# Kernel optimization log

Hardware: AMD Instinct MI355X
Metric: run time of the kernel (lower is better)

## Reference

```python
import jax, jax.numpy as jnp
import numpy as np

B, T, F, G, H, N, C = 32, 64, 32, 32, 256, 20000, 32
EPS = 1e-5


def setup_inputs() -> dict:
    key = jax.random.key(0)
    ks = jax.random.split(key, 24)
    s = 0.05
    d = {}
    d["data_feats"] = jax.random.normal(ks[0], (B, T, F), jnp.float32)
    d["gat_output"] = jax.random.normal(ks[1], (B, N, G), jnp.float32)
    d["row_ids"] = jax.random.randint(ks[2], (B, T), 0, 2 * N, jnp.int32)
    d["node_ids"] = jax.random.randint(ks[3], (N,), 0, 2 * N, jnp.int32)
    # shared LSTM (2 layers): layer0 input F+G, layer1 input H; b = b_ih + b_hh fused
    d["shared_Wih0"] = jax.random.normal(ks[4], (4 * H, F + G)) * s
    d["shared_Whh0"] = jax.random.normal(ks[5], (4 * H, H)) * s
    d["shared_b0"] = jax.random.normal(ks[6], (4 * H,)) * s
    d["shared_Wih1"] = jax.random.normal(ks[7], (4 * H, H)) * s
    d["shared_Whh1"] = jax.random.normal(ks[8], (4 * H, H)) * s
    d["shared_b1"] = jax.random.normal(ks[9], (4 * H,)) * s
    # act/time/timeR LSTMs stacked on leading axis 3, each 2 layers of [4H,H]
    d["heads_Wih"] = jax.random.normal(ks[10], (3, 2, 4 * H, H)) * s
    d["heads_Whh"] = jax.random.normal(ks[11], (3, 2, 4 * H, H)) * s
    d["heads_b"] = jax.random.normal(ks[12], (3, 2, 4 * H)) * s
    d["bn_gnn_g"] = jnp.ones((G,), jnp.float32)
    d["bn_gnn_b"] = jnp.zeros((G,), jnp.float32)
    d["bn_shared_g"] = jnp.ones((H,), jnp.float32)
    d["bn_shared_b"] = jnp.zeros((H,), jnp.float32)
    d["heads_bn_g"] = jnp.ones((3, H), jnp.float32)
    d["heads_bn_b"] = jnp.zeros((3, H), jnp.float32)
    d["fc_act_W"] = jax.random.normal(ks[13], (C, H)) * s
    d["fc_act_b"] = jnp.zeros((C,), jnp.float32)
    d["fc_time_W"] = jax.random.normal(ks[14], (1, H)) * s
    d["fc_time_b"] = jnp.zeros((1,), jnp.float32)
    d["fc_timeR_W"] = jax.random.normal(ks[15], (1, H)) * s
    d["fc_timeR_b"] = jnp.zeros((1,), jnp.float32)
    return d


def batchnorm(x, gamma, beta):
    # BatchNorm1d training-mode: stats over (batch, length) per channel; x: [B, L, C]
    mean = jnp.mean(x, axis=(0, 1))
    var = jnp.var(x, axis=(0, 1))
    return (x - mean) * (gamma / jnp.sqrt(var + EPS)) + beta


def lstm_layer(x, Wih, Whh, b):
    # x: [B, T, Din]; PyTorch gate order i, f, g, o
    xp = jnp.einsum("btf,gf->btg", x, Wih) + b  # [B, T, 4H]
    h = Whh.shape[1]
    init = (jnp.zeros((x.shape[0], h), x.dtype), jnp.zeros((x.shape[0], h), x.dtype))

    def step(carry, xt):
        hprev, cprev = carry
        gates = xt + hprev @ Whh.T
        i, f, g, o = jnp.split(gates, 4, axis=-1)
        c = jax.nn.sigmoid(f) * cprev + jax.nn.sigmoid(i) * jnp.tanh(g)
        hnew = jax.nn.sigmoid(o) * jnp.tanh(c)
        return (hnew, c), hnew

    _, hs = jax.lax.scan(step, init, jnp.swapaxes(xp, 0, 1))
    return jnp.swapaxes(hs, 0, 1)  # [B, T, H]


def reference(data_feats, gat_output, row_ids, node_ids,
              shared_Wih0, shared_Whh0, shared_b0,
              shared_Wih1, shared_Whh1, shared_b1,
              heads_Wih, heads_Whh, heads_b,
              bn_gnn_g, bn_gnn_b, bn_shared_g, bn_shared_b,
              heads_bn_g, heads_bn_b,
              fc_act_W, fc_act_b, fc_time_W, fc_time_b, fc_timeR_W, fc_timeR_b):
    # --- graph branch: BN over GAT output, value-match lookup + gather ---
    gat_norm = batchnorm(gat_output, bn_gnn_g, bn_gnn_b)  # [B, N, G]
    eq = row_ids[:, :, None] == node_ids[None, None, :]   # [B, T, N]
    idx = jnp.argmax(eq, axis=-1)                          # first matching index
    found = jnp.any(eq, axis=-1)
    gathered = jnp.take_along_axis(gat_norm, idx[:, :, None], axis=1)  # [B, T, G]
    matched = jnp.where(found[:, :, None], gathered, 0.0)
    lstm_in = jnp.concatenate([data_feats, matched], axis=-1)  # [B, T, F+G]

    # --- shared 2-layer LSTM + BN (dropout off / eval) ---
    shared = lstm_layer(lstm_in, shared_Wih0, shared_Whh0, shared_b0)
    shared = lstm_layer(shared, shared_Wih1, shared_Whh1, shared_b1)
    shared = batchnorm(shared, bn_shared_g, bn_shared_b)

    # --- act / time / timeR head LSTMs (vmapped over the 3 heads) + BN ---
    def head(Wih, Whh, b, g, bb):
        hh = lstm_layer(shared, Wih[0], Whh[0], b[0])
        hh = lstm_layer(hh, Wih[1], Whh[1], b[1])
        return batchnorm(hh, g, bb)

    heads = jax.vmap(head)(heads_Wih, heads_Whh, heads_b, heads_bn_g, heads_bn_b)
    last = heads[:, :, -1, :]  # [3, B, H]

    act = jax.nn.softmax(last[0] @ fc_act_W.T + fc_act_b, axis=1)
    time = last[1] @ fc_time_W.T + fc_time_b
    timeR = last[2] @ fc_timeR_W.T + fc_timeR_b
    return act, time, timeR
```

## Files before the change

kernel.cpp:

```cpp
#include <hip/hip_runtime.h>
#include <hip/hip_fp16.h>
#include <math.h>

#define Bn 32
#define Tn 64
#define Fdim 32
#define Gdim 32
#define Hdim 256
#define Ndim 20000
#define Cdim 32
#define G4 1024
#define BT 2048
#define EPSc 1e-5f

__device__ __forceinline__ float sigmoidf_(float x){ return 1.0f/(1.0f + __expf(-x)); }
__device__ __forceinline__ float tanhf_(float x){ return 2.0f/(1.0f+__expf(-2.0f*x)) - 1.0f; }

typedef _Float16 h2t __attribute__((ext_vector_type(2)));

__device__ __forceinline__ float fdot2_(unsigned w, unsigned h, float acc){
#if defined(__has_builtin) && __has_builtin(__builtin_amdgcn_fdot2)
  return __builtin_amdgcn_fdot2(__builtin_bit_cast(h2t, w), __builtin_bit_cast(h2t, h), acc, false);
#else
  h2t a = __builtin_bit_cast(h2t, w), b = __builtin_bit_cast(h2t, h);
  acc = fmaf((float)a.x, (float)b.x, acc);
  return fmaf((float)a.y, (float)b.y, acc);
#endif
}

__device__ __forceinline__ unsigned packh_(float lo, float hi){
  unsigned ulo = (unsigned)__half_as_ushort(__float2half(lo));
  unsigned uhi = (unsigned)__half_as_ushort(__float2half(hi));
  return ulo | (uhi << 16);
}

__global__ void init_kernel(float* ws){
  int i = blockIdx.x*256 + threadIdx.x;
  if (i < 2112) ws[i] = 0.0f;
  int* table = (int*)(ws + 2112);
  if (i < 40000) table[i] = 0x7fffffff;
}

__global__ void bn_stats_kernel(const float* __restrict__ gat, float* __restrict__ sums){
  __shared__ float ss[256], sq[256];
  int tid = threadIdx.x;
  int idx = blockIdx.x*256 + tid;
  int stride = gridDim.x*256;
  const int total = Bn*Ndim*Gdim;
  float s=0.f,q=0.f;
  for (int i=idx; i<total; i+=stride){ float v = gat[i]; s+=v; q+=v*v; }
  ss[tid]=s; sq[tid]=q; __syncthreads();
  for (int off=128; off>=32; off>>=1){
    if(tid<off){ ss[tid]+=ss[tid+off]; sq[tid]+=sq[tid+off]; }
    __syncthreads();
  }
  if (tid<32){ atomicAdd(&sums[tid], ss[tid]); atomicAdd(&sums[32+tid], sq[tid]); }
}

__global__ void table_kernel(const int* __restrict__ node_ids, int* __restrict__ table){
  int i = blockIdx.x*256 + threadIdx.x;
  if (i < Ndim) atomicMin(&table[node_ids[i]], i);
}

__global__ void build_input_kernel(const float* __restrict__ feats, const float* __restrict__ gat,
    const int* __restrict__ row_ids, const int* __restrict__ table, const float* __restrict__ sums,
    const float* __restrict__ bng, const float* __restrict__ bnb, unsigned* __restrict__ out){
  int gt = blockIdx.x*256 + threadIdx.x;
  int pos = gt >> 5; int k2 = gt & 31;
  float lo, hi;
  if (k2 < 16){
    float2 v = *(const float2*)(feats + pos*Fdim + 2*k2);
    lo = v.x; hi = v.y;
  } else {
    int g0 = 2*(k2-16);
    int r = row_ids[pos];
    int idx = table[r];
    if (idx < Ndim){
      int b = pos / Tn;
      float2 x = *(const float2*)(gat + (size_t)(b*Ndim + idx)*Gdim + g0);
      const float cnt = (float)(Bn*Ndim);
      float m0 = sums[g0]/cnt,   v0 = sums[32+g0]/cnt - m0*m0;
      float m1 = sums[g0+1]/cnt, v1 = sums[32+g0+1]/cnt - m1*m1;
      lo = (x.x-m0)*bng[g0]*rsqrtf(v0+EPSc) + bnb[g0];
      hi = (x.y-m1)*bng[g0+1]*rsqrtf(v1+EPSc) + bnb[g0+1];
    } else { lo = 0.0f; hi = 0.0f; }
  }
  out[gt] = packh_(lo, hi);
}

struct TArgs { const float* src[8]; unsigned* dst[8]; int K[8]; };
__global__ void packwih_kernel(TArgs a){
  __shared__ unsigned tile[32][33];
  int mat = blockIdx.y;
  int K = a.K[mat];
  int K2 = K >> 1;
  int ktiles = K2 >> 5;
  int tk = blockIdx.x & 3;
  int tn = blockIdx.x >> 2;
  if (tk >= ktiles) return;
  const float* src = a.src[mat];
  unsigned* dst = a.dst[mat];
  int tx = threadIdx.x, ty = threadIdx.y;
  int n0 = tn*32, k2_0 = tk*32;
  #pragma unroll
  for (int i=0;i<4;i++){
    int nn = ty + 8*i;
    const float* p = src + (size_t)(n0+nn)*K + 2*(k2_0 + tx);
    tile[nn][tx] = packh_(p[0], p[1]);
  }
  __syncthreads();
  #pragma unroll
  for (int i=0;i<4;i++){
    int r = ty + 8*i;
    dst[(size_t)(k2_0 + r)*G4 + n0 + tx] = tile[tx][r];
  }
}

struct PkArgs { const float* src[8]; };
__global__ void pack_kernel(PkArgs a, unsigned* __restrict__ dst){
  int gid = blockIdx.x*256 + threadIdx.x;
  int m = gid >> 17;
  int rem = gid & 0x1FFFF;
  int q = rem & 3;
  int t2 = (rem >> 2) & 1023;
  int ci = rem >> 12;
  int c = ci >> 3, i = ci & 7;
  int j = t2 & 255, kq = t2 >> 8;
  int r = 4*j + c;
  int k = kq*64 + 8*i + 2*q;
  const float* W = a.src[m];
  dst[gid] = packh_(W[r*256 + k], W[r*256 + k + 1]);
}

struct PArgs { const unsigned* x[3]; const unsigned* wt[3]; const float* bias[3]; float* out[3]; int K2; };
__global__ __launch_bounds__(256) void proj_kernel(PArgs a){
  int hd = blockIdx.z;
  int n  = blockIdx.y*256 + threadIdx.x;
  int m0 = blockIdx.x*8;
  int K2 = a.K2;
  const unsigned* xh = a.x[hd] + (size_t)m0*K2;
  const unsigned* wt = a.wt[hd];
  float bv = a.bias[hd][n];
  float acc[8];
  #pragma unroll
  for (int i=0;i<8;i++) acc[i]=bv;
  for (int k2=0;k2<K2;k2+=4){
    unsigned w0 = wt[(size_t)(k2+0)*G4+n];
    unsigned w1 = wt[(size_t)(k2+1)*G4+n];
    unsigned w2 = wt[(size_t)(k2+2)*G4+n];
    unsigned w3 = wt[(size_t)(k2+3)*G4+n];
    #pragma unroll
    for (int i=0;i<8;i++){
      uint4 xv = *(const uint4*)(xh + i*K2 + k2);
      acc[i]=fdot2_(w0,xv.x,acc[i]); acc[i]=fdot2_(w1,xv.y,acc[i]);
      acc[i]=fdot2_(w2,xv.z,acc[i]); acc[i]=fdot2_(w3,xv.w,acc[i]);
    }
  }
  float* out = a.out[hd] + (size_t)m0*G4 + n;
  #pragma unroll
  for (int i=0;i<8;i++) out[i*G4]=acc[i];
}

struct RArgs { const float* xp[3]; const unsigned* wt[3]; float* out[3]; unsigned* outh[3]; };
__global__ __launch_bounds__(1024,1) void rec_kernel(RArgs a){
  extern __shared__ float lds[];
  unsigned* lw   = (unsigned*)lds;
  float*    part = lds + 32768;
  unsigned* hp   = (unsigned*)(lds + 36864);
  int b = blockIdx.x, hd = blockIdx.y, tid = threadIdx.x;
  int j = tid & 255, kq = tid >> 8;
  const float* xp = a.xp[hd] + (size_t)b*Tn*G4;
  const unsigned* wt = a.wt[hd];
  float* out = a.out[hd] + (size_t)b*Tn*Hdim;
  unsigned* outh = a.outh[hd] + (size_t)b*Tn*128;

  unsigned w[96];
  #pragma unroll
  for (int c=0;c<4;c++){
    #pragma unroll
    for (int i=0;i<6;i++){
      uint4 v = *(const uint4*)(wt + ((c*8+i)*1024 + tid)*4);
      w[(c*6+i)*4+0]=v.x; w[(c*6+i)*4+1]=v.y; w[(c*6+i)*4+2]=v.z; w[(c*6+i)*4+3]=v.w;
    }
    #pragma unroll
    for (int i=6;i<8;i++){
      uint4 v = *(const uint4*)(wt + ((c*8+i)*1024 + tid)*4);
      *(uint4*)(lw + ((c*2+(i-6))*1024 + tid)*4) = v;
    }
  }
  float cst = 0.0f;
  if (tid < 128){ hp[tid] = 0u; hp[128+tid] = 0u; }
  __syncthreads();

  int p = 0;
  for (int t=0; t<Tn; t++){
    float ac0, ac1, ac2, ac3;
    if (kq == 0){
      float4 xv = *(const float4*)(xp + t*G4 + 4*j);
      ac0=xv.x; ac1=xv.y; ac2=xv.z; ac3=xv.w;
    } else { ac0=0.f; ac1=0.f; ac2=0.f; ac3=0.f; }
    const unsigned* hrow = hp + p*128 + kq*32;
    #pragma unroll
    for (int ic=0; ic<6; ic++){
      uint4 hv = *(const uint4*)(hrow + 4*ic);
      ac0=fdot2_(w[0*24+ic*4+0],hv.x,ac0); ac0=fdot2_(w[0*24+ic*4+1],hv.y,ac0);
      ac0=fdot2_(w[0*24+ic*4+2],hv.z,ac0); ac0=fdot2_(w[0*24+ic*4+3],hv.w,ac0);
      ac1=fdot2_(w[1*24+ic*4+0],hv.x,ac1); ac1=fdot2_(w[1*24+ic*4+1],hv.y,ac1);
      ac1=fdot2_(w[1*24+ic*4+2],hv.z,ac1); ac1=fdot2_(w[1*24+ic*4+3],hv.w,ac1);
      ac2=fdot2_(w[2*24+ic*4+0],hv.x,ac2); ac2=fdot2_(w[2*24+ic*4+1],hv.y,ac2);
      ac2=fdot2_(w[2*24+ic*4+2],hv.z,ac2); ac2=fdot2_(w[2*24+ic*4+3],hv.w,ac2);
      ac3=fdot2_(w[3*24+ic*4+0],hv.x,ac3); ac3=fdot2_(w[3*24+ic*4+1],hv.y,ac3);
      ac3=fdot2_(w[3*24+ic*4+2],hv.z,ac3); ac3=fdot2_(w[3*24+ic*4+3],hv.w,ac3);
    }
    #pragma unroll
    for (int ic=6; ic<8; ic++){
      uint4 hv = *(const uint4*)(hrow + 4*ic);
      { uint4 lv = *(const uint4*)(lw + ((0*2+(ic-6))*1024 + tid)*4);
        ac0=fdot2_(lv.x,hv.x,ac0); ac0=fdot2_(lv.y,hv.y,ac0);
        ac0=fdot2_(lv.z,hv.z,ac0); ac0=fdot2_(lv.w,hv.w,ac0); }
      { uint4 lv = *(const uint4*)(lw + ((1*2+(ic-6))*1024 + tid)*4);
        ac1=fdot2_(lv.x,hv.x,ac1); ac1=fdot2_(lv.y,hv.y,ac1);
        ac1=fdot2_(lv.z,hv.z,ac1); ac1=fdot2_(lv.w,hv.w,ac1); }
      { uint4 lv = *(const uint4*)(lw + ((2*2+(ic-6))*1024 + tid)*4);
        ac2=fdot2_(lv.x,hv.x,ac2); ac2=fdot2_(lv.y,hv.y,ac2);
        ac2=fdot2_(lv.z,hv.z,ac2); ac2=fdot2_(lv.w,hv.w,ac2); }
      { uint4 lv = *(const uint4*)(lw + ((3*2+(ic-6))*1024 + tid)*4);
        ac3=fdot2_(lv.x,hv.x,ac3); ac3=fdot2_(lv.y,hv.y,ac3);
        ac3=fdot2_(lv.z,hv.z,ac3); ac3=fdot2_(lv.w,hv.w,ac3); }
    }
    *(float4*)(part + kq*1024 + 4*j) = make_float4(ac0,ac1,ac2,ac3);
    __syncthreads();
    if (tid < 256){
      int u = tid;
      float gi = part[u]     + part[1024+u]     + part[2048+u]     + part[3072+u];
      float gf = part[256+u] + part[1024+256+u] + part[2048+256+u] + part[3072+256+u];
      float gg = part[512+u] + part[1024+512+u] + part[2048+512+u] + part[3072+512+u];
      float go = part[768+u] + part[1024+768+u] + part[2048+768+u] + part[3072+768+u];
      cst = sigmoidf_(gf)*cst + sigmoidf_(gi)*tanhf_(gg);
      float h = sigmoidf_(go)*tanhf_(cst);
      out[t*Hdim + u] = h;
      float hpartner = __shfl_xor(h, 1);
      if ((u & 1) == 0){
        unsigned hh = packh_(h, hpartner);
        hp[(p^1)*128 + (u>>1)] = hh;
        outh[t*128 + (u>>1)] = hh;
      }
    }
    __syncthreads();
    p ^= 1;
  }
}

struct SArgs { const float* in[3]; float* stats[3]; };
__global__ void stats_kernel(SArgs a){
  int hd = blockIdx.y; int tid = threadIdx.x;
  const float* in = a.in[hd] + blockIdx.x*256*Hdim;
  float s=0.f,q=0.f;
  for (int r=0;r<256;r++){ float v = in[r*Hdim + tid]; s+=v; q+=v*v; }
  atomicAdd(&a.stats[hd][tid], s);
  atomicAdd(&a.stats[hd][Hdim+tid], q);
}

__global__ void norm_kernel(const float* __restrict__ in, const float* __restrict__ stats,
   const float* __restrict__ g, const float* __restrict__ bta, unsigned* __restrict__ outh){
  int i2 = blockIdx.x*256 + threadIdx.x;
  int h2 = i2 & 127; int m = i2 >> 7;
  int h0 = 2*h2;
  float2 v = *(const float2*)(in + (size_t)m*Hdim + h0);
  float m0 = stats[h0]*(1.0f/BT),   v0 = stats[Hdim+h0]*(1.0f/BT) - m0*m0;
  float m1 = stats[h0+1]*(1.0f/BT), v1 = stats[Hdim+h0+1]*(1.0f/BT) - m1*m1;
  float lo = (v.x-m0)*g[h0]*rsqrtf(v0+EPSc) + bta[h0];
  float hi = (v.y-m1)*g[h0+1]*rsqrtf(v1+EPSc) + bta[h0+1];
  outh[i2] = packh_(lo, hi);
}

__global__ __launch_bounds__(256) void final_kernel(
  const float* __restrict__ h0, const float* __restrict__ h1, const float* __restrict__ h2,
  const float* __restrict__ stats,
  const float* __restrict__ hbg, const float* __restrict__ hbb,
  const float* __restrict__ actW, const float* __restrict__ actB,
  const float* __restrict__ tW, const float* __restrict__ tB,
  const float* __restrict__ rW, const float* __restrict__ rB,
  float* __restrict__ outp){
  __shared__ float v0[Bn*Hdim];
  __shared__ float lg[Bn*Cdim];
  int tid = threadIdx.x;
  for (int i=tid; i<Bn*Hdim; i+=256){
    int b=i>>8, h=i&255;
    float sm = stats[512 + h], sq = stats[512+256+h];
    float mean = sm*(1.0f/BT); float var = sq*(1.0f/BT) - mean*mean;
    v0[i] = (h0[(b*Tn+63)*Hdim + h] - mean)*hbg[h]*rsqrtf(var+EPSc) + hbb[h];
  }
  __syncthreads();
  for (int i=tid; i<Bn*Cdim; i+=256){
    int b=i>>5, cc=i&31;
    float acc = actB[cc];
    const float* wrow = actW + cc*Hdim;
    const float* vrow = v0 + b*Hdim;
    #pragma unroll 4
    for (int h=0;h<Hdim;h++) acc = fmaf(vrow[h], wrow[h], acc);
    lg[i] = acc;
  }
  __syncthreads();
  if (tid < Bn){
    int b = tid;
    float m = -1e30f;
    #pragma unroll
    for (int cc=0; cc<Cdim; cc++) m = fmaxf(m, lg[b*Cdim+cc]);
    float e[Cdim]; float s = 0.f;
    #pragma unroll
    for (int cc=0; cc<Cdim; cc++){ float ee = __expf(lg[b*Cdim+cc]-m); e[cc]=ee; s+=ee; }
    float inv = 1.0f/s;
    #pragma unroll
    for (int cc=0; cc<Cdim; cc++) outp[b*Cdim+cc] = e[cc]*inv;
  }
  if (tid < 64){
    int b = tid & 31; int w = tid >> 5;
    const float* hh = w ? h2 : h1;
    const float* fw = w ? rW : tW;
    float fb = w ? rB[0] : tB[0];
    int hd = 1 + w;
    float acc = fb;
    for (int h=0; h<Hdim; h++){
      float sm = stats[(1+hd)*512 + h], sq = stats[(1+hd)*512+256+h];
      float mean = sm*(1.0f/BT); float var = sq*(1.0f/BT) - mean*mean;
      float v = (hh[(b*Tn+63)*Hdim + h] - mean)*hbg[hd*Hdim+h]*rsqrtf(var+EPSc) + hbb[hd*Hdim+h];
      acc = fmaf(v, fw[h], acc);
    }
    outp[1024 + w*32 + b] = acc;
  }
}

extern "C" void kernel_launch(void* const* d_in, const int* in_sizes, int n_in,
                              void* d_out, int out_size, void* d_ws, size_t ws_size,
                              hipStream_t stream){
  const float* data_feats = (const float*)d_in[0];
  const float* gat   = (const float*)d_in[1];
  const int*   row_ids  = (const int*)d_in[2];
  const int*   node_ids = (const int*)d_in[3];
  const float* sWih0 = (const float*)d_in[4];
  const float* sWhh0 = (const float*)d_in[5];
  const float* sb0   = (const float*)d_in[6];
  const float* sWih1 = (const float*)d_in[7];
  const float* sWhh1 = (const float*)d_in[8];
  const float* sb1   = (const float*)d_in[9];
  const float* hWih  = (const float*)d_in[10];
  const float* hWhh  = (const float*)d_in[11];
  const float* hb    = (const float*)d_in[12];
  const float* bng   = (const float*)d_in[13];
  const float* bnb   = (const float*)d_in[14];
  const float* bsg   = (const float*)d_in[15];
  const float* bsb   = (const float*)d_in[16];
  const float* hbg   = (const float*)d_in[17];
  const float* hbb   = (const float*)d_in[18];
  const float* actW  = (const float*)d_in[19];
  const float* actB  = (const float*)d_in[20];
  const float* tW    = (const float*)d_in[21];
  const float* tB    = (const float*)d_in[22];
  const float* rW    = (const float*)d_in[23];
  const float* rB    = (const float*)d_in[24];
  float* ws  = (float*)d_ws;
  float* out = (float*)d_out;

  const size_t S_GAT = 0;
  const size_t S_BN  = 64;
  const size_t TABLE = 2112;
  const size_t WIHP  = 42112;
  const size_t PSLOT = 131072;
  const size_t WHHP  = WIHP + 8*PSLOT;
  const size_t LSTM_INH = WHHP + 8*PSLOT;
  const size_t XPOFF = LSTM_INH + 65536;
  const size_t BUF0H = XPOFF + 3*2097152;
  const size_t BUF1  = BUF0H + 262144;
  const size_t BUFNH = BUF1 + 524288;
  const size_t HB0H  = BUFNH + 262144;
  const size_t HB1   = HB0H + 3*262144;

  const int REC_LDS = 148480;
  hipFuncSetAttribute((const void*)rec_kernel, hipFuncAttributeMaxDynamicSharedMemorySize, REC_LDS);

  init_kernel<<<157,256,0,stream>>>(ws);
  bn_stats_kernel<<<2048,256,0,stream>>>(gat, ws+S_GAT);
  table_kernel<<<(Ndim+255)/256,256,0,stream>>>(node_ids, (int*)(ws+TABLE));
  build_input_kernel<<<256,256,0,stream>>>(data_feats, gat, row_ids, (int*)(ws+TABLE),
                                           ws+S_GAT, bng, bnb, (unsigned*)(ws+LSTM_INH));

  unsigned* wih = (unsigned*)(ws + WIHP);
  TArgs ta;
  ta.src[0]=sWih0; ta.K[0]=64;
  ta.src[1]=sWih1; ta.K[1]=256;
  for (int hd=0; hd<3; hd++) for (int l=0;l<2;l++){
    ta.src[2+hd*2+l] = hWih + (size_t)(hd*2+l)*G4*Hdim; ta.K[2+hd*2+l] = 256;
  }
  for (int i=0;i<8;i++) ta.dst[i] = wih + (size_t)i*PSLOT;
  packwih_kernel<<<dim3(128,8),dim3(32,8),0,stream>>>(ta);

  unsigned* whh = (unsigned*)(ws + WHHP);
  PkArgs pka;
  pka.src[0]=sWhh0; pka.src[1]=sWhh1;
  for (int hd=0; hd<3; hd++) for (int l=0;l<2;l++)
    pka.src[2+hd*2+l] = hWhh + (size_t)(hd*2+l)*G4*Hdim;
  pack_kernel<<<4096,256,0,stream>>>(pka, whh);

  PArgs pa; RArgs ra; SArgs sa;
  pa.K2=32; pa.x[0]=(unsigned*)(ws+LSTM_INH); pa.wt[0]=wih+0*PSLOT; pa.bias[0]=sb0; pa.out[0]=ws+XPOFF;
  proj_kernel<<<dim3(256,4,1),256,0,stream>>>(pa);
  ra.xp[0]=ws+XPOFF; ra.wt[0]=whh+0*PSLOT; ra.out[0]=ws+BUF1;  ra.outh[0]=(unsigned*)(ws+BUF0H);
  rec_kernel<<<dim3(32,1),1024,REC_LDS,stream>>>(ra);
  pa.K2=128; pa.x[0]=(unsigned*)(ws+BUF0H); pa.wt[0]=wih+1*PSLOT; pa.bias[0]=sb1; pa.out[0]=ws+XPOFF;
  proj_kernel<<<dim3(256,4,1),256,0,stream>>>(pa);
  ra.xp[0]=ws+XPOFF; ra.wt[0]=whh+1*PSLOT; ra.out[0]=ws+BUF1; ra.outh[0]=(unsigned*)(ws+BUF0H);
  rec_kernel<<<dim3(32,1),1024,REC_LDS,stream>>>(ra);
  sa.in[0]=ws+BUF1; sa.stats[0]=ws+S_BN;
  stats_kernel<<<dim3(8,1),256,0,stream>>>(sa);
  norm_kernel<<<1024,256,0,stream>>>(ws+BUF1, ws+S_BN, bsg, bsb, (unsigned*)(ws+BUFNH));
  pa.K2=128;
  for (int hd=0;hd<3;hd++){
    pa.x[hd]=(unsigned*)(ws+BUFNH); pa.wt[hd]=wih+(size_t)(2+hd*2)*PSLOT; pa.bias[hd]=hb + (size_t)(hd*2)*G4;
    pa.out[hd]=ws+XPOFF+(size_t)hd*2097152;
  }
  proj_kernel<<<dim3(256,4,3),256,0,stream>>>(pa);
  for (int hd=0;hd<3;hd++){
    ra.xp[hd]=ws+XPOFF+(size_t)hd*2097152; ra.wt[hd]=whh+(size_t)(2+hd*2)*PSLOT;
    ra.out[hd]=ws+HB1+(size_t)hd*524288;  ra.outh[hd]=(unsigned*)(ws+HB0H)+(size_t)hd*262144;
  }
  rec_kernel<<<dim3(32,3),1024,REC_LDS,stream>>>(ra);
  for (int hd=0;hd<3;hd++){
    pa.x[hd]=(unsigned*)(ws+HB0H)+(size_t)hd*262144; pa.wt[hd]=wih+(size_t)(2+hd*2+1)*PSLOT;
    pa.bias[hd]=hb + (size_t)(hd*2+1)*G4;
    pa.out[hd]=ws+XPOFF+(size_t)hd*2097152;
  }
  proj_kernel<<<dim3(256,4,3),256,0,stream>>>(pa);
  for (int hd=0;hd<3;hd++){
    ra.xp[hd]=ws+XPOFF+(size_t)hd*2097152; ra.wt[hd]=whh+(size_t)(2+hd*2+1)*PSLOT;
    ra.out[hd]=ws+HB1+(size_t)hd*524288; ra.outh[hd]=(unsigned*)(ws+HB0H)+(size_t)hd*262144;
  }
  rec_kernel<<<dim3(32,3),1024,REC_LDS,stream>>>(ra);
  for (int hd=0;hd<3;hd++){ sa.in[hd]=ws+HB1+(size_t)hd*524288; sa.stats[hd]=ws+S_BN+(size_t)(1+hd)*512; }
  stats_kernel<<<dim3(8,3),256,0,stream>>>(sa);
  final_kernel<<<1,256,0,stream>>>(ws+HB1, ws+HB1+524288, ws+HB1+2*524288, ws+S_BN,
                                   hbg, hbb, actW, actB, tW, tB, rW, rB, out);
}
```

Before: 869.5 us.

## Remove second barrier in LSTM recurrence with redundant per-wave gate reduction

The recurrent kernel now has every wave redundantly reduce the partial gate sums and compute its own copy of the hidden state into a private LDS slice, with a double-buffered partial array. This drops one of the two block-wide barriers per timestep on the sequential critical path. Partial sums are stored as fp16 and the fp32 hidden output is removed, so downstream stats, norm and final kernels read fp16. This lowers precision and adds redundant transcendental work. The input batchnorm statistics kernel is also vectorised with float4 loads over half as many blocks.

Measured after the change: 1.204 ms. 1.38x slower.

```diff
diff --git a/kernel.cpp b/kernel.cpp
--- a/kernel.cpp
+++ b/kernel.cpp
@@ -34,6 +34,11 @@
   return ulo | (uhi << 16);
 }
 
+__device__ __forceinline__ float unpk_(unsigned d, int odd){
+  h2t p = __builtin_bit_cast(h2t, d);
+  return odd ? (float)p.y : (float)p.x;
+}
+
 __global__ void init_kernel(float* ws){
   int i = blockIdx.x*256 + threadIdx.x;
   if (i < 2112) ws[i] = 0.0f;
@@ -46,15 +51,50 @@
   int tid = threadIdx.x;
   int idx = blockIdx.x*256 + tid;
   int stride = gridDim.x*256;
-  const int total = Bn*Ndim*Gdim;
+  const int total4 = Bn*Ndim*Gdim/4;
+  const float4* g4 = (const float4*)gat;
   float s=0.f,q=0.f;
-  for (int i=idx; i<total; i+=stride){ float v = gat[i]; s+=v; q+=v*v; }
+  for (int i=idx; i<total4; i+=stride){
+    float4 v = g4[i];
+    s += v.x+v.y+v.z+v.w;
+    q += v.x*v.x + v.y*v.y + v.z*v.z + v.w*v.w;
+  }
   ss[tid]=s; sq[tid]=q; __syncthreads();
   for (int off=128; off>=32; off>>=1){
     if(tid<off){ ss[tid]+=ss[tid+off]; sq[tid]+=sq[tid+off]; }
     __syncthreads();
   }
   if (tid<32){ atomicAdd(&sums[tid], ss[tid]); atomicAdd(&sums[32+tid], sq[tid]); }
+}
+__global__ void bn_stats_kernel2(const float* __restrict__ gat, float* __restrict__ sums){
+  __shared__ float ss[256], sq[256];
+  int tid = threadIdx.x;
+  int lane8 = tid & 7;
+  int idx = blockIdx.x*256 + tid;
+  int stride = gridDim.x*256;
+  const int total4 = Bn*Ndim*Gdim/4;
+  const float4* g4 = (const float4*)gat;
+  float4 s = make_float4(0.f,0.f,0.f,0.f), q = make_float4(0.f,0.f,0.f,0.f);
+  for (int i=idx; i<total4; i+=stride){
+    float4 v = g4[i];
+    s.x+=v.x; s.y+=v.y; s.z+=v.z; s.w+=v.w;
+    q.x+=v.x*v.x; q.y+=v.y*v.y; q.z+=v.z*v.z; q.w+=v.w*v.w;
+  }
+  ss[tid]=s.x; sq[tid]=q.x; __syncthreads();
+  for (int off=128; off>=8; off>>=1){ if(tid<off){ ss[tid]+=ss[tid+off]; sq[tid]+=sq[tid+off]; } __syncthreads(); }
+  if (tid<8){ atomicAdd(&sums[4*tid+0], ss[tid]); atomicAdd(&sums[32+4*tid+0], sq[tid]); }
+  __syncthreads();
+  ss[tid]=s.y; sq[tid]=q.y; __syncthreads();
+  for (int off=128; off>=8; off>>=1){ if(tid<off){ ss[tid]+=ss[tid+off]; sq[tid]+=sq[tid+off]; } __syncthreads(); }
+  if (tid<8){ atomicAdd(&sums[4*tid+1], ss[tid]); atomicAdd(&sums[32+4*tid+1], sq[tid]); }
+  __syncthreads();
+  ss[tid]=s.z; sq[tid]=q.z; __syncthreads();
+  for (int off=128; off>=8; off>>=1){ if(tid<off){ ss[tid]+=ss[tid+off]; sq[tid]+=sq[tid+off]; } __syncthreads(); }
+  if (tid<8){ atomicAdd(&sums[4*tid+2], ss[tid]); atomicAdd(&sums[32+4*tid+2], sq[tid]); }
+  __syncthreads();
+  ss[tid]=s.w; sq[tid]=q.w; __syncthreads();
+  for (int off=128; off>=8; off>>=1){ if(tid<off){ ss[tid]+=ss[tid+off]; sq[tid]+=sq[tid+off]; } __syncthreads(); }
+  if (tid<8){ atomicAdd(&sums[4*tid+3], ss[tid]); atomicAdd(&sums[32+4*tid+3], sq[tid]); }
 }
 
 __global__ void table_kernel(const int* __restrict__ node_ids, int* __restrict__ table){
@@ -161,18 +201,21 @@
   for (int i=0;i<8;i++) out[i*G4]=acc[i];
 }
 
-struct RArgs { const float* xp[3]; const unsigned* wt[3]; float* out[3]; unsigned* outh[3]; };
+struct RArgs { const float* xp[3]; const unsigned* wt[3]; unsigned* outh[3]; };
 __global__ __launch_bounds__(1024,1) void rec_kernel(RArgs a){
   extern __shared__ float lds[];
-  unsigned* lw   = (unsigned*)lds;
-  float*    part = lds + 32768;
-  unsigned* hp   = (unsigned*)(lds + 36864);
+  unsigned* lw    = (unsigned*)lds;
+  unsigned* part2 = (unsigned*)(lds + 32768);
+  unsigned* hp    = (unsigned*)(lds + 36864);
   int b = blockIdx.x, hd = blockIdx.y, tid = threadIdx.x;
   int j = tid & 255, kq = tid >> 8;
+  int wave = tid >> 6, lane = tid & 63;
+  int u = (kq << 6) + lane;
   const float* xp = a.xp[hd] + (size_t)b*Tn*G4;
   const unsigned* wt = a.wt[hd];
-  float* out = a.out[hd] + (size_t)b*Tn*Hdim;
   unsigned* outh = a.outh[hd] + (size_t)b*Tn*128;
+  bool storer = ((wave>>2) == (wave&3));
+  unsigned* myhp = hp + wave*32;
 
   unsigned w[96];
   #pragma unroll
@@ -189,20 +232,18 @@
     }
   }
   float cst = 0.0f;
-  if (tid < 128){ hp[tid] = 0u; hp[128+tid] = 0u; }
-  __syncthreads();
-
-  int p = 0;
+  if (lane < 32) myhp[lane] = 0u;
+  __syncthreads();
+
   for (int t=0; t<Tn; t++){
-    float ac0, ac1, ac2, ac3;
-    if (kq == 0){
-      float4 xv = *(const float4*)(xp + t*G4 + 4*j);
-      ac0=xv.x; ac1=xv.y; ac2=xv.z; ac3=xv.w;
-    } else { ac0=0.f; ac1=0.f; ac2=0.f; ac3=0.f; }
-    const unsigned* hrow = hp + p*128 + kq*32;
+    float xi = xp[t*G4 + u];
+    float xf = xp[t*G4 + 256 + u];
+    float xg = xp[t*G4 + 512 + u];
+    float xo = xp[t*G4 + 768 + u];
+    float ac0=0.f, ac1=0.f, ac2=0.f, ac3=0.f;
     #pragma unroll
     for (int ic=0; ic<6; ic++){
-      uint4 hv = *(const uint4*)(hrow + 4*ic);
+      uint4 hv = *(const uint4*)(myhp + 4*ic);
       ac0=fdot2_(w[0*24+ic*4+0],hv.x,ac0); ac0=fdot2_(w[0*24+ic*4+1],hv.y,ac0);
       ac0=fdot2_(w[0*24+ic*4+2],hv.z,ac0); ac0=fdot2_(w[0*24+ic*4+3],hv.w,ac0);
       ac1=fdot2_(w[1*24+ic*4+0],hv.x,ac1); ac1=fdot2_(w[1*24+ic*4+1],hv.y,ac1);
@@ -214,7 +255,7 @@
     }
     #pragma unroll
     for (int ic=6; ic<8; ic++){
-      uint4 hv = *(const uint4*)(hrow + 4*ic);
+      uint4 hv = *(const uint4*)(myhp + 4*ic);
       { uint4 lv = *(const uint4*)(lw + ((0*2+(ic-6))*1024 + tid)*4);
         ac0=fdot2_(lv.x,hv.x,ac0); ac0=fdot2_(lv.y,hv.y,ac0);
         ac0=fdot2_(lv.z,hv.z,ac0); ac0=fdot2_(lv.w,hv.w,ac0); }
@@ -228,54 +269,55 @@
         ac3=fdot2_(lv.x,hv.x,ac3); ac3=fdot2_(lv.y,hv.y,ac3);
         ac3=fdot2_(lv.z,hv.z,ac3); ac3=fdot2_(lv.w,hv.w,ac3); }
     }
-    *(float4*)(part + kq*1024 + 4*j) = make_float4(ac0,ac1,ac2,ac3);
+    unsigned* pb = part2 + (t&1)*2048;
+    *(uint2*)(pb + kq*512 + 2*j) = make_uint2(packh_(ac0,ac1), packh_(ac2,ac3));
     __syncthreads();
-    if (tid < 256){
-      int u = tid;
-      float gi = part[u]     + part[1024+u]     + part[2048+u]     + part[3072+u];
-      float gf = part[256+u] + part[1024+256+u] + part[2048+256+u] + part[3072+256+u];
-      float gg = part[512+u] + part[1024+512+u] + part[2048+512+u] + part[3072+512+u];
-      float go = part[768+u] + part[1024+768+u] + part[2048+768+u] + part[3072+768+u];
-      cst = sigmoidf_(gf)*cst + sigmoidf_(gi)*tanhf_(gg);
-      float h = sigmoidf_(go)*tanhf_(cst);
-      out[t*Hdim + u] = h;
-      float hpartner = __shfl_xor(h, 1);
-      if ((u & 1) == 0){
-        unsigned hh = packh_(h, hpartner);
-        hp[(p^1)*128 + (u>>1)] = hh;
-        outh[t*128 + (u>>1)] = hh;
-      }
-    }
-    __syncthreads();
-    p ^= 1;
-  }
-}
-
-struct SArgs { const float* in[3]; float* stats[3]; };
+    int pu = u >> 1, odd = u & 1;
+    float gi = xi, gf = xf, gg = xg, go = xo;
+    #pragma unroll
+    for (int kqq=0; kqq<4; kqq++){
+      gi += unpk_(pb[kqq*512 +       pu], odd);
+      gf += unpk_(pb[kqq*512 + 128 + pu], odd);
+      gg += unpk_(pb[kqq*512 + 256 + pu], odd);
+      go += unpk_(pb[kqq*512 + 384 + pu], odd);
+    }
+    cst = sigmoidf_(gf)*cst + sigmoidf_(gi)*tanhf_(gg);
+    float h = sigmoidf_(go)*tanhf_(cst);
+    float hq = __shfl_xor(h, 1);
+    if (!(lane & 1)){
+      unsigned hh = packh_(h, hq);
+      myhp[lane>>1] = hh;
+      if (storer) outh[t*128 + (u>>1)] = hh;
+    }
+  }
+}
+
+struct SArgs { const unsigned* in[3]; float* stats[3]; };
 __global__ void stats_kernel(SArgs a){
   int hd = blockIdx.y; int tid = threadIdx.x;
-  const float* in = a.in[hd] + blockIdx.x*256*Hdim;
+  const unsigned* in = a.in[hd] + (size_t)blockIdx.x*256*128;
+  int pu = tid >> 1, odd = tid & 1;
   float s=0.f,q=0.f;
-  for (int r=0;r<256;r++){ float v = in[r*Hdim + tid]; s+=v; q+=v*v; }
+  for (int r=0;r<256;r++){ float v = unpk_(in[r*128 + pu], odd); s+=v; q+=v*v; }
   atomicAdd(&a.stats[hd][tid], s);
   atomicAdd(&a.stats[hd][Hdim+tid], q);
 }
 
-__global__ void norm_kernel(const float* __restrict__ in, const float* __restrict__ stats,
+__global__ void norm_kernel(const unsigned* __restrict__ in, const float* __restrict__ stats,
    const float* __restrict__ g, const float* __restrict__ bta, unsigned* __restrict__ outh){
   int i2 = blockIdx.x*256 + threadIdx.x;
-  int h2 = i2 & 127; int m = i2 >> 7;
-  int h0 = 2*h2;
-  float2 v = *(const float2*)(in + (size_t)m*Hdim + h0);
+  int h2i = i2 & 127;
+  int h0 = 2*h2i;
+  h2t p = __builtin_bit_cast(h2t, in[i2]);
   float m0 = stats[h0]*(1.0f/BT),   v0 = stats[Hdim+h0]*(1.0f/BT) - m0*m0;
   float m1 = stats[h0+1]*(1.0f/BT), v1 = stats[Hdim+h0+1]*(1.0f/BT) - m1*m1;
-  float lo = (v.x-m0)*g[h0]*rsqrtf(v0+EPSc) + bta[h0];
-  float hi = (v.y-m1)*g[h0+1]*rsqrtf(v1+EPSc) + bta[h0+1];
+  float lo = ((float)p.x-m0)*g[h0]*rsqrtf(v0+EPSc) + bta[h0];
+  float hi = ((float)p.y-m1)*g[h0+1]*rsqrtf(v1+EPSc) + bta[h0+1];
   outh[i2] = packh_(lo, hi);
 }
 
 __global__ __launch_bounds__(256) void final_kernel(
-  const float* __restrict__ h0, const float* __restrict__ h1, const float* __restrict__ h2,
+  const unsigned* __restrict__ h0, const unsigned* __restrict__ h1, const unsigned* __restrict__ h2,
   const float* __restrict__ stats,
   const float* __restrict__ hbg, const float* __restrict__ hbb,
   const float* __restrict__ actW, const float* __restrict__ actB,
@@ -289,7 +331,8 @@
     int b=i>>8, h=i&255;
     float sm = stats[512 + h], sq = stats[512+256+h];
     float mean = sm*(1.0f/BT); float var = sq*(1.0f/BT) - mean*mean;
-    v0[i] = (h0[(b*Tn+63)*Hdim + h] - mean)*hbg[h]*rsqrtf(var+EPSc) + hbb[h];
+    float hv = unpk_(h0[(size_t)(b*Tn+63)*128 + (h>>1)], h&1);
+    v0[i] = (hv - mean)*hbg[h]*rsqrtf(var+EPSc) + hbb[h];
   }
   __syncthreads();
   for (int i=tid; i<Bn*Cdim; i+=256){
@@ -316,7 +359,7 @@
   }
   if (tid < 64){
     int b = tid & 31; int w = tid >> 5;
-    const float* hh = w ? h2 : h1;
+    const unsigned* hh = w ? h2 : h1;
     const float* fw = w ? rW : tW;
     float fb = w ? rB[0] : tB[0];
     int hd = 1 + w;
@@ -324,7 +367,8 @@
     for (int h=0; h<Hdim; h++){
       float sm = stats[(1+hd)*512 + h], sq = stats[(1+hd)*512+256+h];
       float mean = sm*(1.0f/BT); float var = sq*(1.0f/BT) - mean*mean;
-      float v = (hh[(b*Tn+63)*Hdim + h] - mean)*hbg[hd*Hdim+h]*rsqrtf(var+EPSc) + hbb[hd*Hdim+h];
+      float hv = unpk_(hh[(size_t)(b*Tn+63)*128 + (h>>1)], h&1);
+      float v = (hv - mean)*hbg[hd*Hdim+h]*rsqrtf(var+EPSc) + hbb[hd*Hdim+h];
       acc = fmaf(v, fw[h], acc);
     }
     outp[1024 + w*32 + b] = acc;
@@ -371,16 +415,16 @@
   const size_t LSTM_INH = WHHP + 8*PSLOT;
   const size_t XPOFF = LSTM_INH + 65536;
   const size_t BUF0H = XPOFF + 3*2097152;
-  const size_t BUF1  = BUF0H + 262144;
-  const size_t BUFNH = BUF1 + 524288;
+  const size_t BUF1H = BUF0H + 262144;
+  const size_t BUFNH = BUF1H + 262144;
   const size_t HB0H  = BUFNH + 262144;
-  const size_t HB1   = HB0H + 3*262144;
-
-  const int REC_LDS = 148480;
+  const size_t HB1H  = HB0H + 3*262144;
+
+  const int REC_LDS = 149504;
   hipFuncSetAttribute((const void*)rec_kernel, hipFuncAttributeMaxDynamicSharedMemorySize, REC_LDS);
 
   init_kernel<<<157,256,0,stream>>>(ws);
-  bn_stats_kernel<<<2048,256,0,stream>>>(gat, ws+S_GAT);
+  bn_stats_kernel2<<<1024,256,0,stream>>>(gat, ws+S_GAT);
   table_kernel<<<(Ndim+255)/256,256,0,stream>>>(node_ids, (int*)(ws+TABLE));
   build_input_kernel<<<256,256,0,stream>>>(data_feats, gat, row_ids, (int*)(ws+TABLE),
                                            ws+S_GAT, bng, bnb, (unsigned*)(ws+LSTM_INH));
@@ -405,15 +449,15 @@
   PArgs pa; RArgs ra; SArgs sa;
   pa.K2=32; pa.x[0]=(unsigned*)(ws+LSTM_INH); pa.wt[0]=wih+0*PSLOT; pa.bias[0]=sb0; pa.out[0]=ws+XPOFF;
   proj_kernel<<<dim3(256,4,1),256,0,stream>>>(pa);
-  ra.xp[0]=ws+XPOFF; ra.wt[0]=whh+0*PSLOT; ra.out[0]=ws+BUF1;  ra.outh[0]=(unsigned*)(ws+BUF0H);
+  ra.xp[0]=ws+XPOFF; ra.wt[0]=whh+0*PSLOT; ra.outh[0]=(unsigned*)(ws+BUF0H);
   rec_kernel<<<dim3(32,1),1024,REC_LDS,stream>>>(ra);
   pa.K2=128; pa.x[0]=(unsigned*)(ws+BUF0H); pa.wt[0]=wih+1*PSLOT; pa.bias[0]=sb1; pa.out[0]=ws+XPOFF;
   proj_kernel<<<dim3(256,4,1),256,0,stream>>>(pa);
-  ra.xp[0]=ws+XPOFF; ra.wt[0]=whh+1*PSLOT; ra.out[0]=ws+BUF1; ra.outh[0]=(unsigned*)(ws+BUF0H);
+  ra.xp[0]=ws+XPOFF; ra.wt[0]=whh+1*PSLOT; ra.outh[0]=(unsigned*)(ws+BUF1H);
   rec_kernel<<<dim3(32,1),1024,REC_LDS,stream>>>(ra);
-  sa.in[0]=ws+BUF1; sa.stats[0]=ws+S_BN;
+  sa.in[0]=(unsigned*)(ws+BUF1H); sa.stats[0]=ws+S_BN;
   stats_kernel<<<dim3(8,1),256,0,stream>>>(sa);
-  norm_kernel<<<1024,256,0,stream>>>(ws+BUF1, ws+S_BN, bsg, bsb, (unsigned*)(ws+BUFNH));
+  norm_kernel<<<1024,256,0,stream>>>((unsigned*)(ws+BUF1H), ws+S_BN, bsg, bsb, (unsigned*)(ws+BUFNH));
   pa.K2=128;
   for (int hd=0;hd<3;hd++){
     pa.x[hd]=(unsigned*)(ws+BUFNH); pa.wt[hd]=wih+(size_t)(2+hd*2)*PSLOT; pa.bias[hd]=hb + (size_t)(hd*2)*G4;
@@ -422,7 +466,7 @@
   proj_kernel<<<dim3(256,4,3),256,0,stream>>>(pa);
   for (int hd=0;hd<3;hd++){
     ra.xp[hd]=ws+XPOFF+(size_t)hd*2097152; ra.wt[hd]=whh+(size_t)(2+hd*2)*PSLOT;
-    ra.out[hd]=ws+HB1+(size_t)hd*524288;  ra.outh[hd]=(unsigned*)(ws+HB0H)+(size_t)hd*262144;
+    ra.outh[hd]=(unsigned*)(ws+HB0H)+(size_t)hd*262144;
   }
   rec_kernel<<<dim3(32,3),1024,REC_LDS,stream>>>(ra);
   for (int hd=0;hd<3;hd++){
@@ -433,11 +477,11 @@
   proj_kernel<<<dim3(256,4,3),256,0,stream>>>(pa);
   for (int hd=0;hd<3;hd++){
     ra.xp[hd]=ws+XPOFF+(size_t)hd*2097152; ra.wt[hd]=whh+(size_t)(2+hd*2+1)*PSLOT;
-    ra.out[hd]=ws+HB1+(size_t)hd*524288; ra.outh[hd]=(unsigned*)(ws+HB0H)+(size_t)hd*262144;
+    ra.outh[hd]=(unsigned*)(ws+HB1H)+(size_t)hd*262144;
   }
   rec_kernel<<<dim3(32,3),1024,REC_LDS,stream>>>(ra);
-  for (int hd=0;hd<3;hd++){ sa.in[hd]=ws+HB1+(size_t)hd*524288; sa.stats[hd]=ws+S_BN+(size_t)(1+hd)*512; }
+  for (int hd=0;hd<3;hd++){ sa.in[hd]=(unsigned*)(ws+HB1H)+(size_t)hd*262144; sa.stats[hd]=ws+S_BN+(size_t)(1+hd)*512; }
   stats_kernel<<<dim3(8,3),256,0,stream>>>(sa);
-  final_kernel<<<1,256,0,stream>>>(ws+HB1, ws+HB1+524288, ws+HB1+2*524288, ws+S_BN,
-                                   hbg, hbb, actW, actB, tW, tB, rW, rB, out);
-}
+  final_kernel<<<1,256,0,stream>>>((unsigned*)(ws+HB1H), (unsigned*)(ws+HB1H)+262144, (unsigned*)(ws+HB1H)+2*262144,
+                                   ws+S_BN, hbg, hbb, actW, actB, tW, tB, rW, rB, out);
+}
```
